# Kernel optimization log

Hardware: AMD Instinct MI355X
Metric: run time of the kernel (lower is better)

## Reference

```python
import jax, jax.numpy as jnp
import numpy as np

B, P, M, N, H = 2, 2048, 1024, 16, 64
NEG = 1e10


def setup_inputs() -> dict:
    key = jax.random.key(0)
    ks = jax.random.split(key, 8)
    std = 0.02
    return {
        "x": jax.random.normal(ks[0], (B, P, M), jnp.float32),
        "kernel_query": std * jax.random.normal(ks[1], (N, M, H), jnp.float32),
        "bias_query": jnp.zeros((N, H), jnp.float32),
        "kernel_key": std * jax.random.normal(ks[2], (N, M, H), jnp.float32),
        "bias_key": jnp.zeros((N, H), jnp.float32),
        "kernel_value": std * jax.random.normal(ks[3], (N, M, H), jnp.float32),
        "bias_value": jnp.zeros((N, H), jnp.float32),
        "kernel_out": std * jax.random.normal(ks[4], (N, H, M), jnp.float32),
        "bias_out": jnp.zeros((M,), jnp.float32),
    }


def reference(x, kernel_query, bias_query, kernel_key, bias_key,
              kernel_value, bias_value, kernel_out, bias_out):
    # per-head projections: [b,p,m] x [n,m,h] -> [b,p,n,h]
    q = jnp.einsum('bpm,nmh->bpnh', x, kernel_query) + bias_query
    k = jnp.einsum('bpm,nmh->bpnh', x, kernel_key) + bias_key
    v = jnp.einsum('bpm,nmh->bpnh', x, kernel_value) + bias_value

    # explicit score matrix [b,n,pq,pk]
    scores = jnp.einsum('bqnh,bknh->bnqk', q, k) / jnp.sqrt(jnp.float32(H))
    # faithful reproduction of original (inverted) mask: keep strictly-upper
    # triangle, subtract 1e10 elsewhere
    p = scores.shape[-1]
    mask = jnp.triu(jnp.ones((p, p), scores.dtype), k=1)  # [pq,pk]
    masked = scores * mask - NEG * (1.0 - mask)
    attn = jax.nn.softmax(masked, axis=-1)

    z = jnp.einsum('bknh,bnqk->bqnh', v, attn)
    return jnp.einsum('bqnh,nhm->bqm', z, kernel_out) + bias_out
```

## Files before the change

### kernel.cpp

```cpp
#include <hip/hip_runtime.h>

typedef __attribute__((ext_vector_type(8))) __bf16 bf16x8;
typedef __attribute__((ext_vector_type(4))) float  f32x4;
typedef unsigned short u16;
typedef unsigned int   u32;

__device__ __forceinline__ u16 f2b(float f) {
  u32 u = __builtin_bit_cast(u32, f);
  u32 r = (u + 0x7FFFu + ((u >> 16) & 1u)) >> 16;
  return (u16)r;
}

typedef __attribute__((address_space(3))) void lds_void;
typedef const __attribute__((address_space(1))) void gbl_void;

__device__ __forceinline__ void gload_lds16(const u16* g, u16* l) {
  __builtin_amdgcn_global_load_lds((gbl_void*)g, (lds_void*)l, 16, 0, 0);
}

#define QSCALE 0.18033688011112042f
#define MFIX   4.328085122666891f

__global__ __launch_bounds__(256) void prep_all(const float* __restrict__ x,
                                                const float* __restrict__ wq,
                                                const float* __restrict__ wk,
                                                const float* __restrict__ wv,
                                                const float* __restrict__ wo,
                                                u16* __restrict__ xb,
                                                u16* __restrict__ wbt,
                                                u16* __restrict__ wot) {
  int bid = blockIdx.x;
  int tid = threadIdx.x;
  if (bid < 4096) {
    int i = bid * 256 + tid;
    float4 v = ((const float4*)x)[i];
    ushort4 o;
    o.x = f2b(v.x); o.y = f2b(v.y); o.z = f2b(v.z); o.w = f2b(v.w);
    ((ushort4*)xb)[i] = o;
    return;
  }
  __shared__ float t[64][65];
  int sub = bid - 4096;
  const float* src; u16* dst; int sstride, dstride, r0, c0;
  if (sub < 768) {
    int proj = sub >> 8, rem = sub & 255;
    int ym = rem >> 4, xt = rem & 15;
    src = ((proj == 0) ? wq : (proj == 1) ? wk : wv) + (size_t)ym * 65536;
    dst = wbt + ((size_t)proj << 20) + (size_t)ym * 65536;
    sstride = 64; dstride = 1024; r0 = xt * 64; c0 = 0;
  } else {
    int s2 = sub - 768;
    src = wo; dst = wot;
    sstride = 1024; dstride = 1024;
    r0 = (s2 & 15) * 64; c0 = (s2 >> 4) * 64;
  }
  int rr = tid >> 2, q = tid & 3;
#pragma unroll
  for (int i = 0; i < 4; ++i) {
    float4 v = *(const float4*)&src[(size_t)(r0 + rr) * sstride + c0 + q * 16 + i * 4];
    t[rr][q * 16 + i * 4 + 0] = v.x;
    t[rr][q * 16 + i * 4 + 1] = v.y;
    t[rr][q * 16 + i * 4 + 2] = v.z;
    t[rr][q * 16 + i * 4 + 3] = v.w;
  }
  __syncthreads();
  int cc = rr;
#pragma unroll
  for (int i = 0; i < 4; ++i) {
    ushort4 o;
    o.x = f2b(t[q * 16 + i * 4 + 0][cc]);
    o.y = f2b(t[q * 16 + i * 4 + 1][cc]);
    o.z = f2b(t[q * 16 + i * 4 + 2][cc]);
    o.w = f2b(t[q * 16 + i * 4 + 3][cc]);
    *(ushort4*)&dst[(size_t)(c0 + cc) * dstride + r0 + q * 16 + i * 4] = o;
  }
}

template <int KDIM>
__device__ __forceinline__ void gemm_main(const u16* __restrict__ A,
                                          const u16* __restrict__ Bm,
                                          int R0, int C0,
                                          u16* As, u16* Bs, f32x4 (&acc)[4][4]) {
  int tid = threadIdx.x;
  int w = tid >> 6, l = tid & 63;
  int lr = l & 15, lg = l >> 4;
  int wr = w >> 1, wc = w & 1;
  for (int k0 = 0; k0 < KDIM; k0 += 32) {
#pragma unroll
    for (int i = 0; i < 2; ++i) {
      int t = w * 2 + i;
      gload_lds16(A  + (size_t)(R0 + t * 16 + (l >> 2)) * KDIM + k0 + (l & 3) * 8, &As[t * 512]);
      gload_lds16(Bm + (size_t)(C0 + t * 16 + (l >> 2)) * KDIM + k0 + (l & 3) * 8, &Bs[t * 512]);
    }
    __syncthreads();
    bf16x8 af[4], bfr[4];
#pragma unroll
    for (int mi = 0; mi < 4; ++mi)
      af[mi] = *(const bf16x8*)&As[(wr * 64 + mi * 16 + lr) * 32 + lg * 8];
#pragma unroll
    for (int ni = 0; ni < 4; ++ni)
      bfr[ni] = *(const bf16x8*)&Bs[(wc * 64 + ni * 16 + lr) * 32 + lg * 8];
#pragma unroll
    for (int mi = 0; mi < 4; ++mi)
#pragma unroll
      for (int ni = 0; ni < 4; ++ni)
        acc[mi][ni] = __builtin_amdgcn_mfma_f32_16x16x32_bf16(af[mi], bfr[ni], acc[mi][ni], 0, 0, 0);
    __syncthreads();
  }
}

__global__ __launch_bounds__(256) void gemm_qkv(const u16* __restrict__ xb,
                                                const u16* __restrict__ wbt,
                                                const float* __restrict__ bq,
                                                const float* __restrict__ bk,
                                                const float* __restrict__ bv,
                                                u16* __restrict__ qb,
                                                u16* __restrict__ kbf,
                                                u16* __restrict__ vtb) {
  __shared__ __align__(16) u16 As[128 * 32];
  __shared__ __align__(16) u16 Bs[128 * 32];
  f32x4 acc[4][4];
#pragma unroll
  for (int mi = 0; mi < 4; ++mi)
#pragma unroll
    for (int ni = 0; ni < 4; ++ni) acc[mi][ni] = (f32x4){0.f, 0.f, 0.f, 0.f};

  int bid = blockIdx.x;
  int rt = bid & 31, ct = bid >> 5;
  int R0 = rt * 128, C0 = ct * 128;
  gemm_main<1024>(xb, wbt, R0, C0, As, Bs, acc);

  int tid = threadIdx.x;
  int w = tid >> 6, l = tid & 63;
  int lr = l & 15, lg = l >> 4;
  int wr = w >> 1, wc = w & 1;
#pragma unroll
  for (int ni = 0; ni < 4; ++ni) {
    int col = C0 + wc * 64 + ni * 16 + lr;
    int proj = col >> 10;
    int within = col & 1023;
    int n = within >> 6, h = within & 63;
    const float* bias = (proj == 0) ? bq : (proj == 1 ? bk : bv);
    float badd = bias[within];
    float scl = (proj == 0) ? QSCALE : 1.0f;
#pragma unroll
    for (int mi = 0; mi < 4; ++mi) {
#pragma unroll
      for (int r = 0; r < 4; ++r) {
        int row = R0 + wr * 64 + mi * 16 + lg * 4 + r;
        int b = row >> 11, p = row & 2047;
        int bn = b * 16 + n;
        u16 u = f2b((acc[mi][ni][r] + badd) * scl);
        if (proj == 0)      qb [((size_t)bn * 2048 + p) * 64 + h] = u;
        else if (proj == 1) kbf[((size_t)bn * 2048 + p) * 64 + h] = u;
        else                vtb[(((size_t)bn * 32 + (p >> 6)) * 64 + h) * 64 + (p & 63)] = u;
      }
    }
  }
}

__global__ __launch_bounds__(256) void mean_v(const u16* __restrict__ vtb,
                                              u16* __restrict__ zb) {
  __shared__ float red[4][64];
  int bn = blockIdx.x;
  int w = threadIdx.x >> 6, h = threadIdx.x & 63;
  const u16* base = vtb + (size_t)bn * 131072 + (size_t)h * 64;
  float acc = 0.f;
  for (int pb = w; pb < 32; pb += 4) {
    const u16* r = base + (size_t)pb * 4096;
#pragma unroll
    for (int c = 0; c < 8; ++c) {
      bf16x8 v = *(const bf16x8*)(r + c * 8);
#pragma unroll
      for (int j = 0; j < 8; ++j) acc += (float)v[j];
    }
  }
  red[w][h] = acc;
  __syncthreads();
  if (w == 0) {
    float s = (red[0][h] + red[1][h] + red[2][h] + red[3][h]) * (1.0f / 2048.0f);
    int b = bn >> 4, n = bn & 15;
    zb[((size_t)(b * 2048 + 2047) * 16 + n) * 64 + h] = f2b(s);
  }
}

#define ATTN_STEP(BUFC, MASKED)                                                \
  {                                                                            \
    if (t + 1 < trips) {                                                       \
      gload_lds16(sk,       &Ks[BUFC ^ 1][w * 1024]);                          \
      gload_lds16(sk + 512, &Ks[BUFC ^ 1][w * 1024 + 512]);                    \
      gload_lds16(sv,       &Vs[BUFC ^ 1][w * 1024]);                          \
      gload_lds16(sv + 512, &Vs[BUFC ^ 1][w * 1024 + 512]);                    \
      sk += 4096; sv += 4096;                                                  \
      asm volatile("s_waitcnt vmcnt(4)" ::: "memory");                         \
    } else {                                                                   \
      asm volatile("s_waitcnt vmcnt(0)" ::: "memory");                         \
    }                                                                          \
    __builtin_amdgcn_s_barrier();                                              \
    asm volatile("" ::: "memory");                                             \
    f32x4 sacc[4];                                                             \
    __builtin_amdgcn_s_setprio(1);                                             \
    _Pragma("unroll") for (int nb = 0; nb < 4; ++nb) {                         \
      int row = nb * 16 + lr, sw = row & 7;                                    \
      bf16x8 kf0 = *(const bf16x8*)&Ks[BUFC][row * 64 + ((lg ^ sw) << 3)];     \
      bf16x8 kf1 = *(const bf16x8*)&Ks[BUFC][row * 64 + (((lg + 4) ^ sw) << 3)]; \
      f32x4 s = (f32x4){0.f, 0.f, 0.f, 0.f};                                   \
      s = __builtin_amdgcn_mfma_f32_16x16x32_bf16(qf0, kf0, s, 0, 0, 0);       \
      s = __builtin_amdgcn_mfma_f32_16x16x32_bf16(qf1, kf1, s, 0, 0, 0);       \
      sacc[nb] = s;                                                            \
    }                                                                          \
    __builtin_amdgcn_s_setprio(0);                                             \
    u16 pbv[4][4];                                                             \
    if (MASKED) {                                                              \
      _Pragma("unroll") for (int nb = 0; nb < 4; ++nb) {                       \
        int key = nb * 16 + lr;                                                \
        _Pragma("unroll") for (int r = 0; r < 4; ++r) {                        \
          int qrow = w * 16 + lg * 4 + r;                                      \
          float xv = (key > qrow) ? sacc[nb][r] : -1.0e10f;                    \
          float pe = __builtin_amdgcn_exp2f(xv - MFIX);                        \
          rsum[r] += pe;                                                       \
          pbv[nb][r] = __builtin_bit_cast(u16, (__bf16)pe);                    \
        }                                                                      \
      }                                                                        \
    } else {                                                                   \
      _Pragma("unroll") for (int nb = 0; nb < 4; ++nb)                         \
        _Pragma("unroll") for (int r = 0; r < 4; ++r) {                        \
          float pe = __builtin_amdgcn_exp2f(sacc[nb][r] - MFIX);               \
          rsum[r] += pe;                                                       \
          pbv[nb][r] = __builtin_bit_cast(u16, (__bf16)pe);                    \
        }                                                                      \
    }                                                                          \
    _Pragma("unroll") for (int nb = 0; nb < 4; ++nb)                           \
      _Pragma("unroll") for (int r = 0; r < 4; ++r) {                          \
        int prow = lg * 4 + r;                                                 \
        Plds[w][prow * 64 + ((((nb * 2) + (lr >> 3)) ^ (prow & 7)) << 3) + (lr & 7)] = pbv[nb][r]; \
      }                                                                        \
    asm volatile("s_waitcnt lgkmcnt(0)" ::: "memory");                         \
    __builtin_amdgcn_sched_barrier(0);                                         \
    bf16x8 pf0 = *(const bf16x8*)&Plds[w][lr * 64 + ((lg ^ (lr & 7)) << 3)];   \
    bf16x8 pf1 = *(const bf16x8*)&Plds[w][lr * 64 + (((4 + lg) ^ (lr & 7)) << 3)]; \
    __builtin_amdgcn_s_setprio(1);                                             \
    _Pragma("unroll") for (int hb = 0; hb < 4; ++hb) {                         \
      int row = hb * 16 + lr, sw = row & 7;                                    \
      bf16x8 vf0 = *(const bf16x8*)&Vs[BUFC][row * 64 + ((lg ^ sw) << 3)];     \
      bf16x8 vf1 = *(const bf16x8*)&Vs[BUFC][row * 64 + (((lg + 4) ^ sw) << 3)]; \
      oacc[hb] = __builtin_amdgcn_mfma_f32_16x16x32_bf16(pf0, vf0, oacc[hb], 0, 0, 0); \
      oacc[hb] = __builtin_amdgcn_mfma_f32_16x16x32_bf16(pf1, vf1, oacc[hb], 0, 0, 0); \
    }                                                                          \
    __builtin_amdgcn_s_setprio(0);                                             \
    asm volatile("" ::: "memory");                                             \
    __builtin_amdgcn_s_barrier();                                              \
    ++t;                                                                       \
  }

__global__ __launch_bounds__(256, 4) void attn_kern(const u16* __restrict__ qb,
                                                    const u16* __restrict__ kbf,
                                                    const u16* __restrict__ vtb,
                                                    u16* __restrict__ zb) {
  __shared__ __align__(16) u16 Ks[2][4096];
  __shared__ __align__(16) u16 Vs[2][4096];
  __shared__ __align__(16) u16 Plds[4][1024];

  int bid = blockIdx.x;
  int bn = bid & 31, c = bid >> 5;
  int trips = 32 - c;
  int tid = threadIdx.x;
  int w = tid >> 6, l = tid & 63;
  int lr = l & 15, lg = l >> 4;

  const u16* Q  = qb  + (size_t)bn * 131072;
  const u16* Kp = kbf + (size_t)bn * 131072;
  const u16* Vt = vtb + (size_t)bn * 131072;

  int row0 = w * 16 + (l >> 3), col8 = l & 7;
  int soff = row0 * 64 + ((col8 ^ (row0 & 7)) << 3);

  int q0w = c * 64 + w * 16;
  bf16x8 qf0 = *(const bf16x8*)&Q[(size_t)(q0w + lr) * 64 + lg * 8];
  bf16x8 qf1 = *(const bf16x8*)&Q[(size_t)(q0w + lr) * 64 + 32 + lg * 8];

  float rsum[4];
  f32x4 oacc[4];
#pragma unroll
  for (int r = 0; r < 4; ++r) rsum[r] = 0.0f;
#pragma unroll
  for (int hb = 0; hb < 4; ++hb) oacc[hb] = (f32x4){0.f, 0.f, 0.f, 0.f};

  const u16* sk = Kp + (size_t)c * 4096 + soff;
  const u16* sv = Vt + (size_t)c * 4096 + soff;
  gload_lds16(sk,       &Ks[0][w * 1024]);
  gload_lds16(sk + 512, &Ks[0][w * 1024 + 512]);
  gload_lds16(sv,       &Vs[0][w * 1024]);
  gload_lds16(sv + 512, &Vs[0][w * 1024 + 512]);
  sk += 4096; sv += 4096;

  int t = 0;
  ATTN_STEP(0, true)
  while (t + 1 < trips) {
    ATTN_STEP(1, false)
    ATTN_STEP(0, false)
  }
  if (t < trips) ATTN_STEP(1, false)

#pragma unroll
  for (int r = 0; r < 4; ++r) {
    float v = rsum[r];
    v += __shfl_xor(v, 1);
    v += __shfl_xor(v, 2);
    v += __shfl_xor(v, 4);
    v += __shfl_xor(v, 8);
    rsum[r] = 1.0f / v;
  }
  int b = bn >> 4, n = bn & 15;
#pragma unroll
  for (int hb = 0; hb < 4; ++hb) {
    int h = hb * 16 + lr;
#pragma unroll
    for (int r = 0; r < 4; ++r) {
      int qrow = q0w + lg * 4 + r;
      zb[((size_t)(b * 2048 + qrow) * 16 + n) * 64 + h] = f2b(oacc[hb][r] * rsum[r]);
    }
  }
}

__global__ __launch_bounds__(256) void gemm_out(const u16* __restrict__ zb,
                                                const u16* __restrict__ wot,
                                                const float* __restrict__ bo,
                                                float* __restrict__ out) {
  __shared__ __align__(16) u16 As[128 * 32];
  __shared__ __align__(16) u16 Bs[64 * 32];
  f32x4 acc[4][2];
#pragma unroll
  for (int mi = 0; mi < 4; ++mi)
#pragma unroll
    for (int ni = 0; ni < 2; ++ni) acc[mi][ni] = (f32x4){0.f, 0.f, 0.f, 0.f};

  int bid = (blockIdx.x & 7) * 64 + (blockIdx.x >> 3);
  int rt = bid >> 4, ct = bid & 15;
  int R0 = rt * 128, C0 = ct * 64;

  int tid = threadIdx.x;
  int w = tid >> 6, l = tid & 63;
  int lr = l & 15, lg = l >> 4;
  int wr = w >> 1, wc = w & 1;

  for (int k0 = 0; k0 < 1024; k0 += 32) {
#pragma unroll
    for (int i = 0; i < 2; ++i) {
      int t = w * 2 + i;
      gload_lds16(zb + (size_t)(R0 + t * 16 + (l >> 2)) * 1024 + k0 + (l & 3) * 8, &As[t * 512]);
    }
    gload_lds16(wot + (size_t)(C0 + w * 16 + (l >> 2)) * 1024 + k0 + (l & 3) * 8, &Bs[w * 512]);
    __syncthreads();
    bf16x8 af[4], bfr[2];
#pragma unroll
    for (int mi = 0; mi < 4; ++mi)
      af[mi] = *(const bf16x8*)&As[(wr * 64 + mi * 16 + lr) * 32 + lg * 8];
#pragma unroll
    for (int ni = 0; ni < 2; ++ni)
      bfr[ni] = *(const bf16x8*)&Bs[(wc * 32 + ni * 16 + lr) * 32 + lg * 8];
#pragma unroll
    for (int mi = 0; mi < 4; ++mi)
#pragma unroll
      for (int ni = 0; ni < 2; ++ni)
        acc[mi][ni] = __builtin_amdgcn_mfma_f32_16x16x32_bf16(af[mi], bfr[ni], acc[mi][ni], 0, 0, 0);
    __syncthreads();
  }

#pragma unroll
  for (int ni = 0; ni < 2; ++ni) {
    int col = C0 + wc * 32 + ni * 16 + lr;
    float badd = bo[col];
#pragma unroll
    for (int mi = 0; mi < 4; ++mi) {
#pragma unroll
      for (int r = 0; r < 4; ++r) {
        int row = R0 + wr * 64 + mi * 16 + lg * 4 + r;
        out[(size_t)row * 1024 + col] = acc[mi][ni][r] + badd;
      }
    }
  }
}

extern "C" void kernel_launch(void* const* d_in, const int* in_sizes, int n_in,
                              void* d_out, int out_size, void* d_ws, size_t ws_size,
                              hipStream_t stream) {
  const float* x  = (const float*)d_in[0];
  const float* wq = (const float*)d_in[1];
  const float* bq = (const float*)d_in[2];
  const float* wk = (const float*)d_in[3];
  const float* bk = (const float*)d_in[4];
  const float* wv = (const float*)d_in[5];
  const float* bv = (const float*)d_in[6];
  const float* wo = (const float*)d_in[7];
  const float* bo = (const float*)d_in[8];
  float* out = (float*)d_out;

  char* ws = (char*)d_ws;
  u16* xb  = (u16*)(ws + ((size_t)0 << 20));
  u16* wbt = (u16*)(ws + ((size_t)8 << 20));
  u16* wot = (u16*)(ws + ((size_t)14 << 20));
  u16* qb  = (u16*)(ws + ((size_t)16 << 20));
  u16* kbf = (u16*)(ws + ((size_t)24 << 20));
  u16* vtb = (u16*)(ws + ((size_t)32 << 20));
  u16* zb  = (u16*)(ws + ((size_t)40 << 20));

  prep_all<<<dim3(5120), dim3(256), 0, stream>>>(x, wq, wk, wv, wo, xb, wbt, wot);
  gemm_qkv<<<dim3(32 * 24), dim3(256), 0, stream>>>(xb, wbt, bq, bk, bv, qb, kbf, vtb);
  attn_kern<<<dim3(1024), dim3(256), 0, stream>>>(qb, kbf, vtb, zb);
  mean_v<<<dim3(32), dim3(256), 0, stream>>>(vtb, zb);
  gemm_out<<<dim3(32 * 16), dim3(256), 0, stream>>>(zb, wot, bo, out);
}
```

Measured before the change: 118.2 us.

## Split long causal attention query tiles across two key ranges and combine partials

The heaviest query tiles (the first 16, which see the most key tiles) are now split into two work items over halves of their key range. Each half writes an unnormalized bf16 partial output and a row sum, and a new combine_z kernel adds and normalizes them. This evens out per-block work in the triangular attention workload, at the cost of an extra launch, extra global traffic and bf16 rounding of the partials. The fixed max-shift constant is dropped from the exp2 so the two partials share a common scale, which relies on scores staying small enough not to overflow.

```diff
diff --git a/kernel.cpp b/kernel.cpp
--- a/kernel.cpp
+++ b/kernel.cpp
@@ -19,7 +19,6 @@
 }
 
 #define QSCALE 0.18033688011112042f
-#define MFIX   4.328085122666891f
 
 __global__ __launch_bounds__(256) void prep_all(const float* __restrict__ x,
                                                 const float* __restrict__ wq,
@@ -181,6 +180,30 @@
     float s = (red[0][h] + red[1][h] + red[2][h] + red[3][h]) * (1.0f / 2048.0f);
     int b = bn >> 4, n = bn & 15;
     zb[((size_t)(b * 2048 + 2047) * 16 + n) * 64 + h] = f2b(s);
+  }
+}
+
+__global__ __launch_bounds__(256) void combine_z(const u16* __restrict__ pz,
+                                                 const float* __restrict__ prs,
+                                                 u16* __restrict__ zb) {
+  int bid = blockIdx.x;
+  int bn = bid & 31, c = bid >> 5;
+  int tid = threadIdx.x;
+  int row = tid >> 2, hq = (tid & 3) * 16;
+  size_t t0 = ((size_t)(bn * 16 + c)) * 4096 + row * 64 + hq;
+  size_t t1 = t0 + (size_t)32 * 16 * 4096;
+  int ri = (bn * 16 + c) * 64 + row;
+  float inv = 1.0f / (prs[ri] + prs[ri + 32 * 16 * 64]);
+  int b = bn >> 4, n = bn & 15;
+  u16* dst = zb + ((size_t)(b * 2048 + c * 64 + row) * 16 + n) * 64 + hq;
+#pragma unroll
+  for (int j = 0; j < 16; j += 8) {
+    bf16x8 a = *(const bf16x8*)(pz + t0 + j);
+    bf16x8 bv = *(const bf16x8*)(pz + t1 + j);
+    u16 ov[8];
+#pragma unroll
+    for (int e = 0; e < 8; ++e) ov[e] = f2b(((float)a[e] + (float)bv[e]) * inv);
+    *(bf16x8*)(dst + j) = *(const bf16x8*)ov;
   }
 }
 
@@ -217,7 +240,7 @@
         _Pragma("unroll") for (int r = 0; r < 4; ++r) {                        \
           int qrow = w * 16 + lg * 4 + r;                                      \
           float xv = (key > qrow) ? sacc[nb][r] : -1.0e10f;                    \
-          float pe = __builtin_amdgcn_exp2f(xv - MFIX);                        \
+          float pe = __builtin_amdgcn_exp2f(xv);                               \
           rsum[r] += pe;                                                       \
           pbv[nb][r] = __builtin_bit_cast(u16, (__bf16)pe);                    \
         }                                                                      \
@@ -225,7 +248,7 @@
     } else {                                                                   \
       _Pragma("unroll") for (int nb = 0; nb < 4; ++nb)                         \
         _Pragma("unroll") for (int r = 0; r < 4; ++r) {                        \
-          float pe = __builtin_amdgcn_exp2f(sacc[nb][r] - MFIX);               \
+          float pe = __builtin_amdgcn_exp2f(sacc[nb][r]);                      \
           rsum[r] += pe;                                                       \
           pbv[nb][r] = __builtin_bit_cast(u16, (__bf16)pe);                    \
         }                                                                      \
@@ -256,14 +279,28 @@
 __global__ __launch_bounds__(256, 4) void attn_kern(const u16* __restrict__ qb,
                                                     const u16* __restrict__ kbf,
                                                     const u16* __restrict__ vtb,
-                                                    u16* __restrict__ zb) {
+                                                    u16* __restrict__ zb,
+                                                    u16* __restrict__ pz,
+                                                    float* __restrict__ prs) {
   __shared__ __align__(16) u16 Ks[2][4096];
   __shared__ __align__(16) u16 Vs[2][4096];
   __shared__ __align__(16) u16 Plds[4][1024];
 
   int bid = blockIdx.x;
-  int bn = bid & 31, c = bid >> 5;
-  int trips = 32 - c;
+  int bn = bid & 31, v = bid >> 5;
+  int u = (v < 16) ? (32 + v) : (v - 16);
+  int c, kstart, ktiles, slot;
+  if (u < 32) {
+    c = u >> 1; slot = u & 1;
+    int rem = 32 - c, h0 = (rem + 1) >> 1;
+    if (slot == 0) { kstart = c; ktiles = h0; }
+    else           { kstart = c + h0; ktiles = rem - h0; }
+  } else {
+    c = u - 16; slot = -1; kstart = c; ktiles = 32 - c;
+  }
+  bool domask = (kstart == c);
+  int trips = ktiles;
+
   int tid = threadIdx.x;
   int w = tid >> 6, l = tid & 63;
   int lr = l & 15, lg = l >> 4;
@@ -286,8 +323,8 @@
 #pragma unroll
   for (int hb = 0; hb < 4; ++hb) oacc[hb] = (f32x4){0.f, 0.f, 0.f, 0.f};
 
-  const u16* sk = Kp + (size_t)c * 4096 + soff;
-  const u16* sv = Vt + (size_t)c * 4096 + soff;
+  const u16* sk = Kp + (size_t)kstart * 4096 + soff;
+  const u16* sv = Vt + (size_t)kstart * 4096 + soff;
   gload_lds16(sk,       &Ks[0][w * 1024]);
   gload_lds16(sk + 512, &Ks[0][w * 1024 + 512]);
   gload_lds16(sv,       &Vs[0][w * 1024]);
@@ -295,7 +332,7 @@
   sk += 4096; sv += 4096;
 
   int t = 0;
-  ATTN_STEP(0, true)
+  ATTN_STEP(0, domask)
   while (t + 1 < trips) {
     ATTN_STEP(1, false)
     ATTN_STEP(0, false)
@@ -304,21 +341,40 @@
 
 #pragma unroll
   for (int r = 0; r < 4; ++r) {
-    float v = rsum[r];
-    v += __shfl_xor(v, 1);
-    v += __shfl_xor(v, 2);
-    v += __shfl_xor(v, 4);
-    v += __shfl_xor(v, 8);
-    rsum[r] = 1.0f / v;
-  }
-  int b = bn >> 4, n = bn & 15;
-#pragma unroll
-  for (int hb = 0; hb < 4; ++hb) {
-    int h = hb * 16 + lr;
-#pragma unroll
-    for (int r = 0; r < 4; ++r) {
-      int qrow = q0w + lg * 4 + r;
-      zb[((size_t)(b * 2048 + qrow) * 16 + n) * 64 + h] = f2b(oacc[hb][r] * rsum[r]);
+    float vv = rsum[r];
+    vv += __shfl_xor(vv, 1);
+    vv += __shfl_xor(vv, 2);
+    vv += __shfl_xor(vv, 4);
+    vv += __shfl_xor(vv, 8);
+    rsum[r] = vv;
+  }
+
+  if (slot < 0) {
+    int b = bn >> 4, n = bn & 15;
+#pragma unroll
+    for (int r = 0; r < 4; ++r) rsum[r] = 1.0f / rsum[r];
+#pragma unroll
+    for (int hb = 0; hb < 4; ++hb) {
+      int h = hb * 16 + lr;
+#pragma unroll
+      for (int r = 0; r < 4; ++r) {
+        int qrow = q0w + lg * 4 + r;
+        zb[((size_t)(b * 2048 + qrow) * 16 + n) * 64 + h] = f2b(oacc[hb][r] * rsum[r]);
+      }
+    }
+  } else {
+    u16* pzp = pz + ((size_t)(slot * 32 + bn) * 16 + c) * 4096;
+#pragma unroll
+    for (int hb = 0; hb < 4; ++hb) {
+      int h = hb * 16 + lr;
+#pragma unroll
+      for (int r = 0; r < 4; ++r)
+        pzp[(size_t)(w * 16 + lg * 4 + r) * 64 + h] = f2b(oacc[hb][r]);
+    }
+    if (lr == 0) {
+      float* prp = prs + ((size_t)(slot * 32 + bn) * 16 + c) * 64 + w * 16 + lg * 4;
+#pragma unroll
+      for (int r = 0; r < 4; ++r) prp[r] = rsum[r];
     }
   }
 }
@@ -404,10 +460,13 @@
   u16* kbf = (u16*)(ws + ((size_t)24 << 20));
   u16* vtb = (u16*)(ws + ((size_t)32 << 20));
   u16* zb  = (u16*)(ws + ((size_t)40 << 20));
+  u16*   pz  = (u16*)(ws + ((size_t)0 << 20));
+  float* prs = (float*)(ws + ((size_t)8 << 20));
 
   prep_all<<<dim3(5120), dim3(256), 0, stream>>>(x, wq, wk, wv, wo, xb, wbt, wot);
   gemm_qkv<<<dim3(32 * 24), dim3(256), 0, stream>>>(xb, wbt, bq, bk, bv, qb, kbf, vtb);
-  attn_kern<<<dim3(1024), dim3(256), 0, stream>>>(qb, kbf, vtb, zb);
+  attn_kern<<<dim3(32 * 48), dim3(256), 0, stream>>>(qb, kbf, vtb, zb, pz, prs);
+  combine_z<<<dim3(512), dim3(256), 0, stream>>>(pz, prs, zb);
   mean_v<<<dim3(32), dim3(256), 0, stream>>>(vtb, zb);
   gemm_out<<<dim3(32 * 16), dim3(256), 0, stream>>>(zb, wot, bo, out);
 }
```

Result: no change. 119.4 us (+1.0%).
